# Kernel optimization log

Measured on AMD Instinct MI355X. Metric: run time of the kernel, lower is better.

The kernel has to match this reference:

```python
import jax, jax.numpy as jnp
import numpy as np

NO, NR, E, D = 50000, 2000, 600000, 128
NEG_SLOPE = 0.2


def setup_inputs() -> dict:
    key = jax.random.key(0)
    ks = jax.random.split(key, 16)
    p = lambda k, shape: jax.random.normal(k, shape, dtype=jnp.float32) * 0.05
    return {
        "x_order": jax.random.normal(ks[0], (NO, D), dtype=jnp.float32),
        "x_rider": jax.random.normal(ks[1], (NR, D), dtype=jnp.float32),
        "order_idx": jax.random.randint(ks[2], (E,), 0, NO),
        "rider_idx": jax.random.randint(ks[3], (E,), 0, NR),
        # GATConv layer 1 (order_input_dim=128 -> hidden_dim=128, heads=1)
        "Ws1": p(ks[4], (D, D)), "Wd1": p(ks[5], (D, D)),
        "as1": p(ks[6], (D,)), "ad1": p(ks[7], (D,)), "b1": jnp.zeros((D,), jnp.float32),
        # GATConv layer 2 (hidden_dim=128 -> output_dim=128, heads=1)
        "Ws2": p(ks[8], (D, D)), "Wd2": p(ks[9], (D, D)),
        "as2": p(ks[10], (D,)), "ad2": p(ks[11], (D,)), "b2": jnp.zeros((D,), jnp.float32),
    }


def _segment_softmax(e, seg, num_segments):
    # numerically-stable softmax over edges grouped by destination node
    m = jax.ops.segment_max(e, seg, num_segments=num_segments)
    ex = jnp.exp(e - m[seg])
    s = jax.ops.segment_sum(ex, seg, num_segments=num_segments)
    return ex / (s[seg] + 1e-16)


def _gat_bipartite(x_src, x_dst, oi, ri, Ws, Wd, a_src, a_dst, b, n_dst):
    # PyG GATConv, heads=1, bipartite (src=order, dst=rider), no self-loops
    hs = x_src @ Ws            # [NO, D]
    hd = x_dst @ Wd            # [NR, D]
    alpha_s = hs @ a_src       # [NO]
    alpha_d = hd @ a_dst       # [NR]
    e = jax.nn.leaky_relu(alpha_s[oi] + alpha_d[ri], NEG_SLOPE)  # [E]
    alpha = _segment_softmax(e, ri, n_dst)                        # [E]
    out = jax.ops.segment_sum(alpha[:, None] * hs[oi], ri, num_segments=n_dst)
    return out + b


def reference(x_order, x_rider, order_idx, rider_idx,
              Ws1, Wd1, as1, ad1, b1, Ws2, Wd2, as2, ad2, b2):
    n_rider = x_rider.shape[0]
    # layer 1: update riders; order features pass through
    r1 = jax.nn.relu(_gat_bipartite(x_order, x_rider, order_idx, rider_idx,
                                    Ws1, Wd1, as1, ad1, b1, n_rider))
    o1 = jax.nn.relu(x_order)
    # layer 2
    r2 = _gat_bipartite(o1, r1, order_idx, rider_idx,
                        Ws2, Wd2, as2, ad2, b2, n_rider)
    # per-edge gather-dot-sigmoid scoring
    scores = jnp.sum(o1[order_idx] * r2[rider_idx], axis=1)
    return jax.nn.sigmoid(scores)
```

## Files before the change

### kernel.cpp

```cpp
#include <hip/hip_runtime.h>
#include <hip/hip_fp16.h>
#include <math.h>

#define NO 50000
#define NR 2000
#define NE 600000
#define D  128
#define NEG_SLOPE 0.2f
#define CAP 448
#define SLOT 512
#define NB 256
#define CH ((NE + NB - 1) / NB)

__global__ void precompute_wv(const float* __restrict__ Ws1, const float* __restrict__ as1,
                              const float* __restrict__ Wd1, const float* __restrict__ ad1,
                              const float* __restrict__ Ws2, const float* __restrict__ as2,
                              const float* __restrict__ Wd2, const float* __restrict__ ad2,
                              float* __restrict__ wsv1, float* __restrict__ wdv1,
                              float* __restrict__ wsv2, float* __restrict__ wdv2) {
    int k = threadIdx.x;
    float s1 = 0.f, d1 = 0.f, s2 = 0.f, d2 = 0.f;
    for (int j = 0; j < D; ++j) {
        s1 += Ws1[k * D + j] * as1[j];
        d1 += Wd1[k * D + j] * ad1[j];
        s2 += Ws2[k * D + j] * as2[j];
        d2 += Wd2[k * D + j] * ad2[j];
    }
    wsv1[k] = s1; wdv1[k] = d1; wsv2[k] = s2; wdv2[k] = d2;
}

__global__ void node_prep(const float* __restrict__ x, const float* __restrict__ xr,
                          const float* __restrict__ wsv1, const float* __restrict__ wsv2,
                          const float* __restrict__ wdv1,
                          float* __restrict__ as1o, float* __restrict__ as2o,
                          float* __restrict__ ad1r, __half* __restrict__ x16) {
    int lane = threadIdx.x & 63;
    if (blockIdx.x < NO / 4) {
        int row = blockIdx.x * 4 + (threadIdx.x >> 6);
        float2 xv = ((const float2*)(x + (size_t)row * D))[lane];
        float2 w1 = ((const float2*)wsv1)[lane];
        float2 w2 = ((const float2*)wsv2)[lane];
        float rx0 = fmaxf(xv.x, 0.f), rx1 = fmaxf(xv.y, 0.f);
        ((__half2*)(x16 + (size_t)row * D))[lane] = __floats2half2_rn(xv.x, xv.y);
        float a1 = xv.x * w1.x + xv.y * w1.y;
        float a2 = rx0 * w2.x + rx1 * w2.y;
        for (int off = 32; off; off >>= 1) {
            a1 += __shfl_down(a1, off);
            a2 += __shfl_down(a2, off);
        }
        if (lane == 0) { as1o[row] = a1; as2o[row] = a2; }
    } else {
        int row = (blockIdx.x - NO / 4) * 4 + (threadIdx.x >> 6);
        float2 xv = ((const float2*)(xr + (size_t)row * D))[lane];
        float2 w1 = ((const float2*)wdv1)[lane];
        float a = xv.x * w1.x + xv.y * w1.y;
        for (int off = 32; off; off >>= 1) a += __shfl_down(a, off);
        if (lane == 0) ad1r[row] = a;
    }
}


__global__ void blockhist_kernel(const int* __restrict__ ri, int* __restrict__ blockHist) {
    __shared__ int h[NR];
    int b = blockIdx.x, t = threadIdx.x;
    for (int i = t; i < NR; i += 256) h[i] = 0;
    __syncthreads();
    int lo = b * CH;
    int hi = lo + CH; if (hi > NE) hi = NE;
    for (int i = lo + t; i < hi; i += 256) atomicAdd(&h[ri[i]], 1);
    __syncthreads();
    for (int i = t; i < NR; i += 256) blockHist[(size_t)b * NR + i] = h[i];
}

__global__ void rowscan_kernel(int* __restrict__ blockHist, int* __restrict__ total) {
    int lane = threadIdx.x & 63;
    int r = blockIdx.x * 4 + (threadIdx.x >> 6);
    if (r >= NR) return;
    int b0 = lane * 4;
    int v0 = blockHist[(size_t)(b0 + 0) * NR + r];
    int v1 = blockHist[(size_t)(b0 + 1) * NR + r];
    int v2 = blockHist[(size_t)(b0 + 2) * NR + r];
    int v3 = blockHist[(size_t)(b0 + 3) * NR + r];
    int s = v0 + v1 + v2 + v3;
    int incl = s;
    for (int off = 1; off < 64; off <<= 1) {
        int u = __shfl_up(incl, off);
        if (lane >= off) incl += u;
    }
    int base = incl - s;
    blockHist[(size_t)(b0 + 0) * NR + r] = base;
    blockHist[(size_t)(b0 + 1) * NR + r] = base + v0;
    blockHist[(size_t)(b0 + 2) * NR + r] = base + v0 + v1;
    blockHist[(size_t)(b0 + 3) * NR + r] = base + v0 + v1 + v2;
    int tot = __shfl(incl, 63);
    if (lane == 0) total[r] = tot;
}

__global__ void scatter_kernel(const int* __restrict__ oi, const int* __restrict__ ri,
                               const int* __restrict__ blockHist,
                               int* __restrict__ sOrd) {
    __shared__ int h[NR];
    int b = blockIdx.x, t = threadIdx.x;
    for (int i = t; i < NR; i += 256) h[i] = 0;
    __syncthreads();
    int lo = b * CH;
    int hi = lo + CH; if (hi > NE) hi = NE;
    for (int i = lo + t; i < hi; i += 256) {
        int r = ri[i];
        int rank = atomicAdd(&h[r], 1);
        int pos = r * SLOT + blockHist[(size_t)b * NR + r] + rank;
        sOrd[pos] = oi[i];
    }
}

template <int L>
__global__ void __launch_bounds__(256)
rider_agg(const __half* __restrict__ x16, const float* __restrict__ as_o,
          const float* __restrict__ ad_r,
          const int* __restrict__ cnt, const int* __restrict__ sOrd,
          const float* __restrict__ W, const float* __restrict__ bias,
          const float* __restrict__ wdv2,
          float* __restrict__ ad2r, __half* __restrict__ r216) {
    __shared__ float eL[CAP];
    __shared__ int   sO[CAP];
    __shared__ float red[256];
    __shared__ float red8[256][9];
    __shared__ float tl[D];
    int r = blockIdx.x, t = threadIdx.x;
    int base = r * SLOT, n = cnt[r];
    float ad = ad_r[r];
    int grp = t >> 4, lh = t & 15;

    float ls = 0.f;
    for (int i = t; i < n; i += 256) {
        int o = sOrd[base + i];
        float e = as_o[o] + ad;
        e = (e > 0.f) ? e : NEG_SLOPE * e;
        float ex = __expf(e);
        if (i < CAP) { eL[i] = ex; sO[i] = o; }
        ls += ex;
    }
    red[t] = ls;
    __syncthreads();
    for (int off = 128; off; off >>= 1) {
        if (t < off) red[t] += red[t + off];
        __syncthreads();
    }
    float inv = 1.f / (red[0] + 1e-16f);
    __syncthreads();

    float acc[8];
#pragma unroll
    for (int k = 0; k < 8; ++k) acc[k] = 0.f;
    if (n <= CAP) {
        int i = grp;
        for (; i + 48 < n; i += 64) {
            float a0 = eL[i], a1 = eL[i + 16], a2 = eL[i + 32], a3 = eL[i + 48];
            uint4 h0 = ((const uint4*)(x16 + (size_t)sO[i]      * D))[lh];
            uint4 h1 = ((const uint4*)(x16 + (size_t)sO[i + 16] * D))[lh];
            uint4 h2 = ((const uint4*)(x16 + (size_t)sO[i + 32] * D))[lh];
            uint4 h3 = ((const uint4*)(x16 + (size_t)sO[i + 48] * D))[lh];
            const __half2* p0 = (const __half2*)&h0;
            const __half2* p1 = (const __half2*)&h1;
            const __half2* p2 = (const __half2*)&h2;
            const __half2* p3 = (const __half2*)&h3;
#pragma unroll
            for (int q = 0; q < 4; ++q) {
                float2 f0 = __half22float2(p0[q]);
                float2 f1 = __half22float2(p1[q]);
                float2 f2 = __half22float2(p2[q]);
                float2 f3 = __half22float2(p3[q]);
                if (L == 2) {
                    f0.x = fmaxf(f0.x, 0.f); f0.y = fmaxf(f0.y, 0.f);
                    f1.x = fmaxf(f1.x, 0.f); f1.y = fmaxf(f1.y, 0.f);
                    f2.x = fmaxf(f2.x, 0.f); f2.y = fmaxf(f2.y, 0.f);
                    f3.x = fmaxf(f3.x, 0.f); f3.y = fmaxf(f3.y, 0.f);
                }
                acc[2 * q]     += a0 * f0.x + a1 * f1.x + a2 * f2.x + a3 * f3.x;
                acc[2 * q + 1] += a0 * f0.y + a1 * f1.y + a2 * f2.y + a3 * f3.y;
            }
        }
        for (; i + 16 < n; i += 32) {
            float a0 = eL[i], a1 = eL[i + 16];
            uint4 h0 = ((const uint4*)(x16 + (size_t)sO[i]      * D))[lh];
            uint4 h1 = ((const uint4*)(x16 + (size_t)sO[i + 16] * D))[lh];
            const __half2* p0 = (const __half2*)&h0;
            const __half2* p1 = (const __half2*)&h1;
#pragma unroll
            for (int q = 0; q < 4; ++q) {
                float2 f0 = __half22float2(p0[q]);
                float2 f1 = __half22float2(p1[q]);
                if (L == 2) {
                    f0.x = fmaxf(f0.x, 0.f); f0.y = fmaxf(f0.y, 0.f);
                    f1.x = fmaxf(f1.x, 0.f); f1.y = fmaxf(f1.y, 0.f);
                }
                acc[2 * q]     += a0 * f0.x + a1 * f1.x;
                acc[2 * q + 1] += a0 * f0.y + a1 * f1.y;
            }
        }
        if (i < n) {
            float a0 = eL[i];
            uint4 h0 = ((const uint4*)(x16 + (size_t)sO[i] * D))[lh];
            const __half2* p0 = (const __half2*)&h0;
#pragma unroll
            for (int q = 0; q < 4; ++q) {
                float2 f0 = __half22float2(p0[q]);
                if (L == 2) { f0.x = fmaxf(f0.x, 0.f); f0.y = fmaxf(f0.y, 0.f); }
                acc[2 * q]     += a0 * f0.x;
                acc[2 * q + 1] += a0 * f0.y;
            }
        }
    } else {
        for (int i = grp; i < n; i += 16) {
            float a0; int o;
            if (i < CAP) { a0 = eL[i]; o = sO[i]; }
            else {
                o = sOrd[base + i];
                float e = as_o[o] + ad;
                e = (e > 0.f) ? e : NEG_SLOPE * e;
                a0 = __expf(e);
            }
            uint4 h0 = ((const uint4*)(x16 + (size_t)o * D))[lh];
            const __half2* p0 = (const __half2*)&h0;
#pragma unroll
            for (int q = 0; q < 4; ++q) {
                float2 f0 = __half22float2(p0[q]);
                if (L == 2) { f0.x = fmaxf(f0.x, 0.f); f0.y = fmaxf(f0.y, 0.f); }
                acc[2 * q]     += a0 * f0.x;
                acc[2 * q + 1] += a0 * f0.y;
            }
        }
    }
#pragma unroll
    for (int k = 0; k < 8; ++k) red8[t][k] = acc[k];
    __syncthreads();
    if (t < D) {
        int lh2 = t >> 3, k = t & 7;
        float s = 0.f;
        for (int g = 0; g < 16; ++g) s += red8[g * 16 + lh2][k];
        tl[t] = s * inv;
    }
    __syncthreads();

    int d = t & 127, h = t >> 7;
    float a2 = 0.f;
    for (int k = h * 64; k < h * 64 + 64; ++k) a2 += tl[k] * W[k * D + d];
    red[t] = a2;
    __syncthreads();
    if (L == 1) {
        if (t < 128) red[t] = fmaxf(red[t] + red[t + 128] + bias[t], 0.f) * wdv2[t];
        __syncthreads();
        for (int off = 64; off; off >>= 1) {
            if (t < off) red[t] += red[t + off];
            __syncthreads();
        }
        if (t == 0) ad2r[r] = red[0];
    } else {
        if (t < 128) r216[(size_t)r * D + t] = __float2half(red[t] + red[t + 128] + bias[t]);
    }
}

__global__ void score_edges(const __half* __restrict__ x16, const __half* __restrict__ r216,
                            const int* __restrict__ oi, const int* __restrict__ ri,
                            float* __restrict__ out) {
    int gid = blockIdx.x * blockDim.x + threadIdx.x;
    int e  = gid >> 4;
    int lh = gid & 15;
    if (e >= NE) return;
    int o = oi[e], r = ri[e];
    uint4 hx = ((const uint4*)(x16  + (size_t)o * D))[lh];
    uint4 hr = ((const uint4*)(r216 + (size_t)r * D))[lh];
    float2 a0 = __half22float2(*(const __half2*)&hx.x);
    float2 a1 = __half22float2(*(const __half2*)&hx.y);
    float2 a2 = __half22float2(*(const __half2*)&hx.z);
    float2 a3 = __half22float2(*(const __half2*)&hx.w);
    float2 b0 = __half22float2(*(const __half2*)&hr.x);
    float2 b1 = __half22float2(*(const __half2*)&hr.y);
    float2 b2 = __half22float2(*(const __half2*)&hr.z);
    float2 b3 = __half22float2(*(const __half2*)&hr.w);
    float p = fmaxf(a0.x, 0.f) * b0.x + fmaxf(a0.y, 0.f) * b0.y +
              fmaxf(a1.x, 0.f) * b1.x + fmaxf(a1.y, 0.f) * b1.y +
              fmaxf(a2.x, 0.f) * b2.x + fmaxf(a2.y, 0.f) * b2.y +
              fmaxf(a3.x, 0.f) * b3.x + fmaxf(a3.y, 0.f) * b3.y;
    p += __shfl_xor(p, 8);
    p += __shfl_xor(p, 4);
    p += __shfl_xor(p, 2);
    p += __shfl_xor(p, 1);
    if (lh == 0) out[e] = 1.f / (1.f + __expf(-p));
}

extern "C" void kernel_launch(void* const* d_in, const int* in_sizes, int n_in,
                              void* d_out, int out_size, void* d_ws, size_t ws_size,
                              hipStream_t stream) {
    const float* x_order = (const float*)d_in[0];
    const float* x_rider = (const float*)d_in[1];
    const int*   oi      = (const int*)d_in[2];
    const int*   ri      = (const int*)d_in[3];
    const float* Ws1 = (const float*)d_in[4];
    const float* Wd1 = (const float*)d_in[5];
    const float* as1 = (const float*)d_in[6];
    const float* ad1 = (const float*)d_in[7];
    const float* b1  = (const float*)d_in[8];
    const float* Ws2 = (const float*)d_in[9];
    const float* Wd2 = (const float*)d_in[10];
    const float* as2 = (const float*)d_in[11];
    const float* ad2 = (const float*)d_in[12];
    const float* b2  = (const float*)d_in[13];
    float* out = (float*)d_out;

    char* w = (char*)d_ws;
    float* wsv1 = (float*)w; w += 512;
    float* wdv1 = (float*)w; w += 512;
    float* wsv2 = (float*)w; w += 512;
    float* wdv2 = (float*)w; w += 512;
    float* as1o = (float*)w; w += (size_t)NO * 4;
    float* as2o = (float*)w; w += (size_t)NO * 4;
    float* ad1r = (float*)w; w += (size_t)NR * 4;
    float* ad2r = (float*)w; w += (size_t)NR * 4;
    int* total  = (int*)w;   w += (size_t)NR * 4;
    int* blockHist = (int*)w; w += (size_t)NB * NR * 4;
    int* sOrd   = (int*)w;   w += (size_t)NR * SLOT * 4;
    __half* x16  = (__half*)w; w += (size_t)NO * D * 2;
    __half* r216 = (__half*)w; w += (size_t)NR * D * 2;

    precompute_wv<<<1, 128, 0, stream>>>(Ws1, as1, Wd1, ad1, Ws2, as2, Wd2, ad2,
                                         wsv1, wdv1, wsv2, wdv2);
    node_prep<<<NO / 4 + NR / 4, 256, 0, stream>>>(x_order, x_rider, wsv1, wsv2, wdv1,
                                                   as1o, as2o, ad1r, x16);

    blockhist_kernel<<<NB, 256, 0, stream>>>(ri, blockHist);
    rowscan_kernel<<<NR / 4, 256, 0, stream>>>(blockHist, total);
    scatter_kernel<<<NB, 256, 0, stream>>>(oi, ri, blockHist, sOrd);

    rider_agg<1><<<NR, 256, 0, stream>>>(x16, as1o, ad1r, total, sOrd,
                                         Ws1, b1, wdv2, ad2r, (__half*)0);
    rider_agg<2><<<NR, 256, 0, stream>>>(x16, as2o, ad2r, total, sOrd,
                                         Ws2, b2, (float*)0, (float*)0, r216);
    score_edges<<<(NE * 16 + 255) / 256, 256, 0, stream>>>(x16, r216, oi, ri, out);
}
```

Measured before the change: 227.3 us.

## Split per-rider aggregation into two half-edge blocks plus combine kernel

Each rider's edge list is split across two blocks, each computing partial softmax denominators and weighted feature sums written to global scratch. A new combine kernel per layer sums the two partials, normalizes, and applies the weight matmul and bias. This doubles block count to raise occupancy and shorten the per-block serial gather loop, at the cost of two extra kernel launches and partial-result traffic through global memory.

```diff
diff --git a/kernel.cpp b/kernel.cpp
--- a/kernel.cpp
+++ b/kernel.cpp
@@ -7,7 +7,7 @@
 #define NE 600000
 #define D  128
 #define NEG_SLOPE 0.2f
-#define CAP 448
+#define HCAP 256
 #define SLOT 512
 #define NB 256
 #define CH ((NE + NB - 1) / NB)
@@ -115,29 +115,30 @@
 
 template <int L>
 __global__ void __launch_bounds__(256)
-rider_agg(const __half* __restrict__ x16, const float* __restrict__ as_o,
-          const float* __restrict__ ad_r,
-          const int* __restrict__ cnt, const int* __restrict__ sOrd,
-          const float* __restrict__ W, const float* __restrict__ bias,
-          const float* __restrict__ wdv2,
-          float* __restrict__ ad2r, __half* __restrict__ r216) {
-    __shared__ float eL[CAP];
-    __shared__ int   sO[CAP];
+agg_part(const __half* __restrict__ x16, const float* __restrict__ as_o,
+         const float* __restrict__ ad_r,
+         const int* __restrict__ cnt, const int* __restrict__ sOrd,
+         float* __restrict__ ps, float* __restrict__ pt) {
+    __shared__ float eL[HCAP];
+    __shared__ int   sO[HCAP];
     __shared__ float red[256];
     __shared__ float red8[256][9];
-    __shared__ float tl[D];
-    int r = blockIdx.x, t = threadIdx.x;
-    int base = r * SLOT, n = cnt[r];
+    int b = blockIdx.x, t = threadIdx.x;
+    int r = b >> 1, half = b & 1;
+    int n = cnt[r];
+    int m0 = (n + 1) >> 1;
+    int beg = r * SLOT + (half ? m0 : 0);
+    int m = half ? (n - m0) : m0;
     float ad = ad_r[r];
     int grp = t >> 4, lh = t & 15;
 
     float ls = 0.f;
-    for (int i = t; i < n; i += 256) {
-        int o = sOrd[base + i];
+    for (int i = t; i < m; i += 256) {
+        int o = sOrd[beg + i];
         float e = as_o[o] + ad;
         e = (e > 0.f) ? e : NEG_SLOPE * e;
         float ex = __expf(e);
-        if (i < CAP) { eL[i] = ex; sO[i] = o; }
+        if (i < HCAP) { eL[i] = ex; sO[i] = o; }
         ls += ex;
     }
     red[t] = ls;
@@ -146,15 +147,14 @@
         if (t < off) red[t] += red[t + off];
         __syncthreads();
     }
-    float inv = 1.f / (red[0] + 1e-16f);
-    __syncthreads();
+    if (t == 0) ps[b] = red[0];
 
     float acc[8];
 #pragma unroll
     for (int k = 0; k < 8; ++k) acc[k] = 0.f;
-    if (n <= CAP) {
+    if (m <= HCAP) {
         int i = grp;
-        for (; i + 48 < n; i += 64) {
+        for (; i + 48 < m; i += 64) {
             float a0 = eL[i], a1 = eL[i + 16], a2 = eL[i + 32], a3 = eL[i + 48];
             uint4 h0 = ((const uint4*)(x16 + (size_t)sO[i]      * D))[lh];
             uint4 h1 = ((const uint4*)(x16 + (size_t)sO[i + 16] * D))[lh];
@@ -180,7 +180,7 @@
                 acc[2 * q + 1] += a0 * f0.y + a1 * f1.y + a2 * f2.y + a3 * f3.y;
             }
         }
-        for (; i + 16 < n; i += 32) {
+        for (; i + 16 < m; i += 32) {
             float a0 = eL[i], a1 = eL[i + 16];
             uint4 h0 = ((const uint4*)(x16 + (size_t)sO[i]      * D))[lh];
             uint4 h1 = ((const uint4*)(x16 + (size_t)sO[i + 16] * D))[lh];
@@ -198,7 +198,7 @@
                 acc[2 * q + 1] += a0 * f0.y + a1 * f1.y;
             }
         }
-        if (i < n) {
+        if (i < m) {
             float a0 = eL[i];
             uint4 h0 = ((const uint4*)(x16 + (size_t)sO[i] * D))[lh];
             const __half2* p0 = (const __half2*)&h0;
@@ -211,11 +211,11 @@
             }
         }
     } else {
-        for (int i = grp; i < n; i += 16) {
+        for (int i = grp; i < m; i += 16) {
             float a0; int o;
-            if (i < CAP) { a0 = eL[i]; o = sO[i]; }
+            if (i < HCAP) { a0 = eL[i]; o = sO[i]; }
             else {
-                o = sOrd[base + i];
+                o = sOrd[beg + i];
                 float e = as_o[o] + ad;
                 e = (e > 0.f) ? e : NEG_SLOPE * e;
                 a0 = __expf(e);
@@ -238,14 +238,28 @@
         int lh2 = t >> 3, k = t & 7;
         float s = 0.f;
         for (int g = 0; g < 16; ++g) s += red8[g * 16 + lh2][k];
-        tl[t] = s * inv;
-    }
-    __syncthreads();
-
+        pt[(size_t)b * D + t] = s;
+    }
+}
+
+template <int L>
+__global__ void __launch_bounds__(256)
+combine(const float* __restrict__ ps, const float* __restrict__ pt,
+        const float* __restrict__ W, const float* __restrict__ bias,
+        const float* __restrict__ wdv2,
+        float* __restrict__ ad2r, __half* __restrict__ r216) {
+    __shared__ float tl[D];
+    __shared__ float red[256];
+    int r = blockIdx.x, t = threadIdx.x;
+    if (t < D) {
+        float inv = 1.f / (ps[2 * r] + ps[2 * r + 1] + 1e-16f);
+        tl[t] = (pt[(size_t)(2 * r) * D + t] + pt[(size_t)(2 * r + 1) * D + t]) * inv;
+    }
+    __syncthreads();
     int d = t & 127, h = t >> 7;
-    float a2 = 0.f;
-    for (int k = h * 64; k < h * 64 + 64; ++k) a2 += tl[k] * W[k * D + d];
-    red[t] = a2;
+    float a = 0.f;
+    for (int k = h * 64; k < h * 64 + 64; ++k) a += tl[k] * W[k * D + d];
+    red[t] = a;
     __syncthreads();
     if (L == 1) {
         if (t < 128) red[t] = fmaxf(red[t] + red[t + 128] + bias[t], 0.f) * wdv2[t];
@@ -318,8 +332,10 @@
     float* ad1r = (float*)w; w += (size_t)NR * 4;
     float* ad2r = (float*)w; w += (size_t)NR * 4;
     int* total  = (int*)w;   w += (size_t)NR * 4;
+    float* ps   = (float*)w; w += (size_t)2 * NR * 4;
     int* blockHist = (int*)w; w += (size_t)NB * NR * 4;
     int* sOrd   = (int*)w;   w += (size_t)NR * SLOT * 4;
+    float* pt   = (float*)w; w += (size_t)2 * NR * D * 4;
     __half* x16  = (__half*)w; w += (size_t)NO * D * 2;
     __half* r216 = (__half*)w; w += (size_t)NR * D * 2;
 
@@ -332,9 +348,9 @@
     rowscan_kernel<<<NR / 4, 256, 0, stream>>>(blockHist, total);
     scatter_kernel<<<NB, 256, 0, stream>>>(oi, ri, blockHist, sOrd);
 
-    rider_agg<1><<<NR, 256, 0, stream>>>(x16, as1o, ad1r, total, sOrd,
-                                         Ws1, b1, wdv2, ad2r, (__half*)0);
-    rider_agg<2><<<NR, 256, 0, stream>>>(x16, as2o, ad2r, total, sOrd,
-                                         Ws2, b2, (float*)0, (float*)0, r216);
+    agg_part<1><<<2 * NR, 256, 0, stream>>>(x16, as1o, ad1r, total, sOrd, ps, pt);
+    combine<1><<<NR, 256, 0, stream>>>(ps, pt, Ws1, b1, wdv2, ad2r, (__half*)0);
+    agg_part<2><<<2 * NR, 256, 0, stream>>>(x16, as2o, ad2r, total, sOrd, ps, pt);
+    combine<2><<<NR, 256, 0, stream>>>(ps, pt, Ws2, b2, (float*)0, (float*)0, r216);
     score_edges<<<(NE * 16 + 255) / 256, 256, 0, stream>>>(x16, r216, oi, ri, out);
 }
```

Measured after the change: 236.2 us. 3.9% more time.
